# Kernel optimization log

Measured on AMD Instinct MI355X. Metric: run time of the kernel, lower is better.

## Reference

```python
import jax, jax.numpy as jnp
import numpy as np
import math

D_MODEL = 1024
NUM_HEADS = 16
HEAD_DIM = D_MODEL // NUM_HEADS


def setup_inputs() -> dict:
    key = jax.random.key(0)
    ks = jax.random.split(key, 10)
    B, Sq, Skv = 2, 2048, 2048
    s = 1.0 / math.sqrt(D_MODEL)
    return {
        "X": jax.random.normal(ks[0], (B, Skv, D_MODEL), jnp.float32),
        "y": jax.random.normal(ks[1], (B, Sq, D_MODEL), jnp.float32),
        "qW": jax.random.normal(ks[2], (D_MODEL, D_MODEL), jnp.float32) * s,
        "qB": jnp.zeros((D_MODEL,), jnp.float32),
        "kW": jax.random.normal(ks[3], (D_MODEL, D_MODEL), jnp.float32) * s,
        "kB": jnp.zeros((D_MODEL,), jnp.float32),
        "vW": jax.random.normal(ks[4], (D_MODEL, D_MODEL), jnp.float32) * s,
        "vB": jnp.zeros((D_MODEL,), jnp.float32),
        "oW": jax.random.normal(ks[5], (D_MODEL, D_MODEL), jnp.float32) * s,
        "oB": jnp.zeros((D_MODEL,), jnp.float32),
    }


def _split_heads(x):
    # (B, S, D) -> (B, H, S, dk)
    B, S, _ = x.shape
    return x.reshape(B, S, NUM_HEADS, HEAD_DIM).transpose(0, 2, 1, 3)


def reference(X, y, qW, qB, kW, kB, vW, vB, oW, oB):
    B = X.shape[0]
    q = _split_heads(y @ qW + qB)   # queries come from y (decoder)
    k = _split_heads(X @ kW + kB)   # keys/values from X (encoder)
    v = _split_heads(X @ vW + vB)
    scale = 1.0 / math.sqrt(HEAD_DIM)
    scores = jnp.einsum("bhqd,bhkd->bhqk", q, k) * scale
    weights = jax.nn.softmax(scores, axis=-1)
    attn = jnp.einsum("bhqk,bhkd->bhqd", weights, v)
    concat = attn.transpose(0, 2, 1, 3).reshape(B, -1, D_MODEL)
    return concat @ oW + oB
```

## Files before the change

kernel.cpp:

```cpp
#include <hip/hip_runtime.h>
#include <hip/hip_bf16.h>
#include <math.h>

typedef __hip_bfloat16 bf16;
typedef __bf16 nbf16;
typedef __bf16 bf16x8 __attribute__((ext_vector_type(8)));
typedef __bf16 bf16x4 __attribute__((ext_vector_type(4)));
typedef float f32x4 __attribute__((ext_vector_type(4)));

#define D_MODEL 1024
#define NHEAD   16
#define HDK     64
#define BATCH   2
#define SEQ     2048
#define QSZ     ((size_t)BATCH * SEQ * D_MODEL)
#define WSZ     ((size_t)D_MODEL * D_MODEL)

__global__ void detect_dtype(const unsigned short* __restrict__ x, int* flag) {
    __shared__ int cnt;
    if (threadIdx.x == 0) cnt = 0;
    __syncthreads();
    int local = 0;
    for (int i = threadIdx.x; i < 4096; i += 256) {
        const unsigned short v = x[i];
        const int e = (v >> 7) & 0xFF;
        if (v == 0 || (e >= 96 && e <= 141)) local++;
    }
    atomicAdd(&cnt, local);
    __syncthreads();
    if (threadIdx.x == 0) *flag = (cnt >= 3600) ? 1 : 0;
}

__device__ __forceinline__ float ldIn(const void* p, size_t i, int isbf16) {
    return isbf16 ? __bfloat162float(((const bf16*)p)[i])
                  : ((const float*)p)[i];
}

__device__ __forceinline__ void gload_lds16(const void* g, void* l) {
    __builtin_amdgcn_global_load_lds(
        (const __attribute__((address_space(1))) void*)g,
        (__attribute__((address_space(3))) void*)l, 16, 0, 0);
}

__global__ void tobf16_xy(const void* __restrict__ X, const void* __restrict__ Y,
                          nbf16* __restrict__ Xb, nbf16* __restrict__ Yb,
                          const int* __restrict__ flagp) {
    const int flag = *flagp;
    const int half = (int)(QSZ / 2048);
    const bool isX = blockIdx.x < half;
    const void* in = isX ? X : Y;
    nbf16* out     = isX ? Xb : Yb;
    const size_t i = ((size_t)(isX ? blockIdx.x : blockIdx.x - half) * 256 +
                      threadIdx.x) * 8;
    if (flag) {
        *(uint4*)(out + i) = *(const uint4*)((const nbf16*)in + i);
    } else {
        const float4 a = *(const float4*)((const float*)in + i);
        const float4 b = *(const float4*)((const float*)in + i + 4);
        bf16x8 v = {(nbf16)a.x, (nbf16)a.y, (nbf16)a.z, (nbf16)a.w,
                    (nbf16)b.x, (nbf16)b.y, (nbf16)b.z, (nbf16)b.w};
        *(bf16x8*)(out + i) = v;
    }
}

__global__ void wtrans4(const void* __restrict__ qW, const void* __restrict__ kW,
                        const void* __restrict__ vW, const void* __restrict__ oW,
                        nbf16* __restrict__ Wt3, nbf16* __restrict__ Wto,
                        const int* __restrict__ flagp) {
    const int flag = *flagp;
    const int z = blockIdx.z;
    const void* W = (z == 0) ? qW : (z == 1) ? kW : (z == 2) ? vW : oW;
    nbf16* Wt = (z == 3) ? Wto : Wt3 + (size_t)z * WSZ;

    __shared__ float T[64][65];
    const int k0 = blockIdx.x * 64, n0 = blockIdx.y * 64;
    #pragma unroll
    for (int i = 0; i < 16; ++i) {
        const int idx = threadIdx.x + i * 256;
        const int r = idx >> 6, c = idx & 63;
        T[r][c] = ldIn(W, (size_t)(k0 + r) * D_MODEL + n0 + c, flag);
    }
    __syncthreads();
    #pragma unroll
    for (int i = 0; i < 16; ++i) {
        const int idx = threadIdx.x + i * 256;
        const int n = idx >> 6, k = idx & 63;
        Wt[(size_t)(n0 + n) * D_MODEL + k0 + k] = (nbf16)T[k][n];
    }
}

#define STAGE128(Albuf, Blbuf, Aptr, Bptr, t)                                  \
{                                                                              \
    const int _k0 = (t) * 64;                                                  \
    _Pragma("unroll")                                                          \
    for (int i = 0; i < 4; ++i) {                                              \
        const int row = i * 32 + wid * 8 + (lane >> 3);                        \
        const int ss  = (lane & 7) ^ (row & 7);                                \
        gload_lds16((Aptr) + (size_t)row * D_MODEL + _k0 + ss * 8,             \
                    (nbf16*)(Albuf) + i * 2048 + wid * 512);                   \
        gload_lds16((Bptr) + (size_t)row * D_MODEL + _k0 + ss * 8,             \
                    (nbf16*)(Blbuf) + i * 2048 + wid * 512);                   \
    }                                                                          \
}

#define GEMM128_LOOP(Al, Bl)                                                   \
    const int NT = D_MODEL / 64;                                               \
    for (int t = 0; t < NT; ++t) {                                             \
        const int cur = t & 1;                                                 \
        if (t + 1 < NT)                                                        \
            STAGE128(&Al[cur ^ 1][0][0], &Bl[cur ^ 1][0][0], Am, Bm, t + 1);   \
        _Pragma("unroll")                                                      \
        for (int kk = 0; kk < 2; ++kk) {                                       \
            bf16x8 af[4], bfr[4];                                              \
            _Pragma("unroll")                                                  \
            for (int mi = 0; mi < 4; ++mi) {                                   \
                const int ar = wr * 64 + mi * 16 + l15;                        \
                const int sl = ((kk << 2) + lg) ^ (ar & 7);                    \
                af[mi] = *(const bf16x8*)((const nbf16*)&Al[cur][ar][0] + sl * 8); \
            }                                                                  \
            _Pragma("unroll")                                                  \
            for (int ni = 0; ni < 4; ++ni) {                                   \
                const int br = wc * 64 + ni * 16 + l15;                        \
                const int sl = ((kk << 2) + lg) ^ (br & 7);                    \
                bfr[ni] = *(const bf16x8*)((const nbf16*)&Bl[cur][br][0] + sl * 8); \
            }                                                                  \
            _Pragma("unroll")                                                  \
            for (int mi = 0; mi < 4; ++mi)                                     \
                _Pragma("unroll")                                              \
                for (int ni = 0; ni < 4; ++ni)                                 \
                    acc[mi][ni] = __builtin_amdgcn_mfma_f32_16x16x32_bf16(     \
                        af[mi], bfr[ni], acc[mi][ni], 0, 0, 0);                \
        }                                                                      \
        __syncthreads();                                                       \
    }

__global__ __launch_bounds__(256, 2) void proj_qkv(
        const nbf16* __restrict__ Xb, const nbf16* __restrict__ Yb,
        const nbf16* __restrict__ Wt3,
        const void* __restrict__ qB, const void* __restrict__ kB,
        const void* __restrict__ vB,
        nbf16* __restrict__ outq, const int* __restrict__ flagp) {
    __shared__ nbf16 Al[2][128][64];
    __shared__ nbf16 Bl[2][128][64];

    const int flag = *flagp;
    const int tid  = threadIdx.x;
    const int wid  = tid >> 6;
    const int lane = tid & 63;
    const int l15  = lane & 15;
    const int lg   = lane >> 4;
    const int wr   = wid >> 1;
    const int wc   = wid & 1;

    const int id = blockIdx.x;
    const int sw = (id & 7) * 96 + (id >> 3);
    const int m0  = (sw & 31) * 128;
    const int ng0 = (sw >> 5) * 128;

    const nbf16* A  = (ng0 < D_MODEL) ? Yb : Xb;
    const nbf16* Bm = Wt3 + (size_t)ng0 * D_MODEL;
    const nbf16* Am = A + (size_t)m0 * D_MODEL;

    f32x4 acc[4][4];
    #pragma unroll
    for (int mi = 0; mi < 4; ++mi)
        #pragma unroll
        for (int ni = 0; ni < 4; ++ni) acc[mi][ni] = (f32x4){0.f, 0.f, 0.f, 0.f};

    STAGE128(&Al[0][0][0], &Bl[0][0][0], Am, Bm, 0);
    __syncthreads();

    GEMM128_LOOP(Al, Bl)

    #pragma unroll
    for (int ni = 0; ni < 4; ++ni) {
        const int n  = ng0 + wc * 64 + ni * 16 + l15;
        const int wh = n >> 10;
        const int nl = n & 1023;
        const void* bp = (wh == 0) ? qB : (wh == 1) ? kB : vB;
        const float bias = ldIn(bp, (size_t)nl, flag);
        nbf16* outp = outq + (size_t)wh * QSZ;
        #pragma unroll
        for (int mi = 0; mi < 4; ++mi) {
            #pragma unroll
            for (int r = 0; r < 4; ++r) {
                const int m = m0 + wr * 64 + mi * 16 + lg * 4 + r;
                const float v = acc[mi][ni][r] + bias;
                const int b = m >> 11, s = m & (SEQ - 1);
                const int h = nl >> 6,  d = nl & (HDK - 1);
                outp[(((size_t)(b * NHEAD + h)) * SEQ + s) * HDK + d] = (nbf16)v;
            }
        }
    }
}

__global__ __launch_bounds__(256, 2) void proj_o(
        const nbf16* __restrict__ A, const nbf16* __restrict__ Wt,
        const void* __restrict__ Braw, void* __restrict__ Cout,
        const int* __restrict__ flagp) {
    __shared__ nbf16 Al[2][128][64];
    __shared__ nbf16 Bl[2][128][64];

    const int flag = *flagp;
    const int tid  = threadIdx.x;
    const int wid  = tid >> 6;
    const int lane = tid & 63;
    const int l15  = lane & 15;
    const int lg   = lane >> 4;
    const int wr   = wid >> 1;
    const int wc   = wid & 1;

    const int id = blockIdx.x;
    const int sw = (id & 7) * 32 + (id >> 3);
    const int m0 = (sw >> 3) * 128;
    const int n0 = (sw & 7) * 128;

    const nbf16* Am = A + (size_t)m0 * D_MODEL;
    const nbf16* Bm = Wt + (size_t)n0 * D_MODEL;

    f32x4 acc[4][4];
    #pragma unroll
    for (int mi = 0; mi < 4; ++mi)
        #pragma unroll
        for (int ni = 0; ni < 4; ++ni) acc[mi][ni] = (f32x4){0.f, 0.f, 0.f, 0.f};

    STAGE128(&Al[0][0][0], &Bl[0][0][0], Am, Bm, 0);
    __syncthreads();

    GEMM128_LOOP(Al, Bl)

    #pragma unroll
    for (int ni = 0; ni < 4; ++ni) {
        const int n = n0 + wc * 64 + ni * 16 + l15;
        const float bias = ldIn(Braw, (size_t)n, flag);
        #pragma unroll
        for (int mi = 0; mi < 4; ++mi) {
            #pragma unroll
            for (int r = 0; r < 4; ++r) {
                const int m = m0 + wr * 64 + mi * 16 + lg * 4 + r;
                const float v = acc[mi][ni][r] + bias;
                if (flag) ((bf16*)Cout)[(size_t)m * D_MODEL + n] = __float2bfloat16(v);
                else      ((float*)Cout)[(size_t)m * D_MODEL + n] = v;
            }
        }
    }
}

__global__ __launch_bounds__(256, 4) void attn_mfma(
        const nbf16* __restrict__ qg, const nbf16* __restrict__ kg,
        const nbf16* __restrict__ vg, nbf16* __restrict__ cg) {
    __shared__ nbf16 VT[2][64][72];
    __shared__ nbf16 PB[4][32][72];

    const int tid  = threadIdx.x;
    const int wid  = tid >> 6;
    const int lane = tid & 63;
    const int l15  = lane & 15;
    const int lg   = lane >> 4;

    const int id = blockIdx.x;
    const int sw = (id & 7) * 64 + (id >> 3);
    const int bh = sw >> 4;
    const int qt = sw & 15;

    const nbf16* qb = qg + (size_t)bh * SEQ * HDK;
    const nbf16* kb = kg + (size_t)bh * SEQ * HDK;
    const nbf16* vb = vg + (size_t)bh * SEQ * HDK;

    const float SCf = 0.125f * 1.44269504088896340736f;

    const int qbase = qt * 128 + wid * 32;
    const nbf16* qpA = qb + (size_t)(qbase + l15) * HDK + lg * 8;
    const nbf16* qpB = qpA + 16 * HDK;
    bf16x8 qfA0 = *(const bf16x8*)qpA;
    bf16x8 qfA1 = *(const bf16x8*)(qpA + 32);
    bf16x8 qfB0 = *(const bf16x8*)qpB;
    bf16x8 qfB1 = *(const bf16x8*)(qpB + 32);
    #pragma unroll
    for (int j = 0; j < 8; ++j) {
        qfA0[j] = (nbf16)((float)qfA0[j] * SCf);
        qfA1[j] = (nbf16)((float)qfA1[j] * SCf);
        qfB0[j] = (nbf16)((float)qfB0[j] * SCf);
        qfB1[j] = (nbf16)((float)qfB1[j] * SCf);
    }

    const bf16x8 ones = {(nbf16)1.f, (nbf16)1.f, (nbf16)1.f, (nbf16)1.f,
                         (nbf16)1.f, (nbf16)1.f, (nbf16)1.f, (nbf16)1.f};

    const int g8 = (tid >> 5) * 8;
    const int p2 = (tid & 31) * 2;

    #define VLOAD(t)                                                           \
        a0 = *(const uint4*)(vb + (size_t)((t) * 64 + p2) * HDK + g8);         \
        a1 = *(const uint4*)(vb + (size_t)((t) * 64 + p2 + 1) * HDK + g8);

    #define VWRITE(buf)                                                        \
    {                                                                          \
        const unsigned short* e0 = (const unsigned short*)&a0;                 \
        const unsigned short* e1 = (const unsigned short*)&a1;                 \
        _Pragma("unroll")                                                      \
        for (int j = 0; j < 8; ++j)                                            \
            *(unsigned int*)&VT[buf][g8 + j][p2] =                             \
                (unsigned int)e0[j] | ((unsigned int)e1[j] << 16);             \
    }

    #define SOFTMAX(st, m2, o, osum, pbrow)                                    \
    do {                                                                       \
        float tmx[4];                                                          \
        _Pragma("unroll")                                                      \
        for (int s_ = 0; s_ < 4; ++s_)                                         \
            tmx[s_] = fmaxf(fmaxf(st[s_][0], st[s_][1]),                       \
                            fmaxf(st[s_][2], st[s_][3]));                      \
        float tm = fmaxf(fmaxf(tmx[0], tmx[1]), fmaxf(tmx[2], tmx[3]));        \
        tm = fmaxf(tm, __shfl_xor(tm, 16, 64));                                \
        tm = fmaxf(tm, __shfl_xor(tm, 32, 64));                                \
        const bool nresc = __all(tm - m2 <= 8.0f);                             \
        const float mref = nresc ? m2 : fmaxf(m2, tm);                         \
        _Pragma("unroll")                                                      \
        for (int s_ = 0; s_ < 4; ++s_) {                                       \
            const float p0 = exp2f(st[s_][0] - mref);                          \
            const float p1 = exp2f(st[s_][1] - mref);                          \
            const float p2_ = exp2f(st[s_][2] - mref);                         \
            const float p3 = exp2f(st[s_][3] - mref);                          \
            bf16x4 pk = {(nbf16)p0, (nbf16)p1, (nbf16)p2_, (nbf16)p3};         \
            *(bf16x4*)((pbrow) + s_ * 16 + lg * 4) = pk;                       \
        }                                                                      \
        if (!nresc) {                                                          \
            const float alpha = exp2f(m2 - mref);                              \
            m2 = mref;                                                         \
            float av[4];                                                       \
            _Pragma("unroll")                                                  \
            for (int r = 0; r < 4; ++r) av[r] = __shfl(alpha, lg * 4 + r, 64); \
            _Pragma("unroll")                                                  \
            for (int i = 0; i < 4; ++i)                                        \
                _Pragma("unroll")                                              \
                for (int r = 0; r < 4; ++r) o[i][r] *= av[r];                  \
            _Pragma("unroll")                                                  \
            for (int r = 0; r < 4; ++r) osum[r] *= av[r];                      \
        }                                                                      \
    } while (0)

    float m2A = -3.0e38f, m2B = -3.0e38f;
    f32x4 oA[4], oB[4], osumA, osumB;
    #pragma unroll
    for (int i = 0; i < 4; ++i) { oA[i] = (f32x4){0,0,0,0}; oB[i] = (f32x4){0,0,0,0}; }
    osumA = (f32x4){0, 0, 0, 0};
    osumB = (f32x4){0, 0, 0, 0};

    const int NT = SEQ / 64;

    {
        uint4 a0, a1;
        VLOAD(0);
        VWRITE(0);
    }
    __syncthreads();

    for (int t = 0; t < NT; ++t) {
        const int cur = t & 1;
        uint4 a0, a1;
        if (t + 1 < NT) VLOAD(t + 1);

        f32x4 stA[4], stB[4];
        const nbf16* kt = kb + (size_t)t * 64 * HDK;
        __builtin_amdgcn_s_setprio(1);
        #pragma unroll
        for (int sub = 0; sub < 4; ++sub) {
            const nbf16* kp = kt + (size_t)(sub * 16 + l15) * HDK + lg * 8;
            const bf16x8 kf0 = *(const bf16x8*)kp;
            const bf16x8 kf1 = *(const bf16x8*)(kp + 32);
            f32x4 a = (f32x4){0, 0, 0, 0};
            a = __builtin_amdgcn_mfma_f32_16x16x32_bf16(kf0, qfA0, a, 0, 0, 0);
            a = __builtin_amdgcn_mfma_f32_16x16x32_bf16(kf1, qfA1, a, 0, 0, 0);
            stA[sub] = a;
            f32x4 b = (f32x4){0, 0, 0, 0};
            b = __builtin_amdgcn_mfma_f32_16x16x32_bf16(kf0, qfB0, b, 0, 0, 0);
            b = __builtin_amdgcn_mfma_f32_16x16x32_bf16(kf1, qfB1, b, 0, 0, 0);
            stB[sub] = b;
        }
        __builtin_amdgcn_s_setprio(0);

        SOFTMAX(stA, m2A, oA, osumA, &PB[wid][l15][0]);
        SOFTMAX(stB, m2B, oB, osumB, &PB[wid][16 + l15][0]);

        __asm__ volatile("s_waitcnt lgkmcnt(0)" ::: "memory");

        const bf16x8 pfA0 = *(const bf16x8*)&PB[wid][l15][lg * 8];
        const bf16x8 pfA1 = *(const bf16x8*)&PB[wid][l15][lg * 8 + 32];
        const bf16x8 pfB0 = *(const bf16x8*)&PB[wid][16 + l15][lg * 8];
        const bf16x8 pfB1 = *(const bf16x8*)&PB[wid][16 + l15][lg * 8 + 32];
        __builtin_amdgcn_s_setprio(1);
        #pragma unroll
        for (int db = 0; db < 4; ++db) {
            const bf16x8 vf0 = *(const bf16x8*)&VT[cur][db * 16 + l15][lg * 8];
            const bf16x8 vf1 = *(const bf16x8*)&VT[cur][db * 16 + l15][lg * 8 + 32];
            oA[db] = __builtin_amdgcn_mfma_f32_16x16x32_bf16(pfA0, vf0, oA[db], 0, 0, 0);
            oA[db] = __builtin_amdgcn_mfma_f32_16x16x32_bf16(pfA1, vf1, oA[db], 0, 0, 0);
            oB[db] = __builtin_amdgcn_mfma_f32_16x16x32_bf16(pfB0, vf0, oB[db], 0, 0, 0);
            oB[db] = __builtin_amdgcn_mfma_f32_16x16x32_bf16(pfB1, vf1, oB[db], 0, 0, 0);
        }
        osumA = __builtin_amdgcn_mfma_f32_16x16x32_bf16(pfA0, ones, osumA, 0, 0, 0);
        osumA = __builtin_amdgcn_mfma_f32_16x16x32_bf16(pfA1, ones, osumA, 0, 0, 0);
        osumB = __builtin_amdgcn_mfma_f32_16x16x32_bf16(pfB0, ones, osumB, 0, 0, 0);
        osumB = __builtin_amdgcn_mfma_f32_16x16x32_bf16(pfB1, ones, osumB, 0, 0, 0);
        __builtin_amdgcn_s_setprio(0);

        if (t + 1 < NT) VWRITE(cur ^ 1);
        __syncthreads();
    }

    const int b = bh >> 4, h = bh & 15;
    #pragma unroll
    for (int db = 0; db < 4; ++db) {
        #pragma unroll
        for (int r = 0; r < 4; ++r) {
            const int qA = qbase + lg * 4 + r;
            cg[((size_t)(b * SEQ + qA)) * D_MODEL + h * HDK + db * 16 + l15] =
                (nbf16)(oA[db][r] / osumA[r]);
            const int qB_ = qbase + 16 + lg * 4 + r;
            cg[((size_t)(b * SEQ + qB_)) * D_MODEL + h * HDK + db * 16 + l15] =
                (nbf16)(oB[db][r] / osumB[r]);
        }
    }
    #undef VLOAD
    #undef VWRITE
    #undef SOFTMAX
}

extern "C" void kernel_launch(void* const* d_in, const int* in_sizes, int n_in,
                              void* d_out, int out_size, void* d_ws, size_t ws_size,
                              hipStream_t stream) {
    const void* X  = d_in[0];
    const void* Y  = d_in[1];
    const void* qW = d_in[2];
    const void* qB = d_in[3];
    const void* kW = d_in[4];
    const void* kB = d_in[5];
    const void* vW = d_in[6];
    const void* vB = d_in[7];
    const void* oW = d_in[8];
    const void* oB = d_in[9];

    nbf16* ws = (nbf16*)d_ws;
    nbf16* qbuf = ws;
    nbf16* kbuf = qbuf + QSZ;
    nbf16* vbuf = kbuf + QSZ;
    nbf16* cbuf = vbuf + QSZ;
    nbf16* Xb   = cbuf + QSZ;
    nbf16* Yb   = Xb + QSZ;
    nbf16* Wt3  = Yb + QSZ;
    nbf16* Wto  = Wt3 + 3 * WSZ;
    int*   flag = (int*)(Wto + WSZ);

    detect_dtype<<<1, 256, 0, stream>>>((const unsigned short*)X, flag);

    tobf16_xy<<<(int)(2 * (QSZ / 2048)), 256, 0, stream>>>(X, Y, Xb, Yb, flag);

    wtrans4<<<dim3(16, 16, 4), 256, 0, stream>>>(qW, kW, vW, oW, Wt3, Wto, flag);

    proj_qkv<<<768, 256, 0, stream>>>(Xb, Yb, Wt3, qB, kB, vB, qbuf, flag);

    attn_mfma<<<512, 256, 0, stream>>>(qbuf, kbuf, vbuf, cbuf);

    proj_o<<<256, 256, 0, stream>>>(cbuf, Wto, oB, d_out, flag);
}
```

Baseline: 285.5 us.

## Stage K tiles into swizzled LDS via async global-to-LDS loads

The attention kernel now double-buffers each 64-row K tile into shared memory with direct global-to-LDS loads and an XOR swizzle. Previously every wave read K fragments straight from global memory, so the four waves of a block each re-fetched the same tile. The K load for the next tile is issued alongside the V prefetch so it overlaps with the current tile's compute. The change adds 16 KB of LDS and lowers the launch-bounds occupancy hint from 4 to 2 blocks per CU, which may reduce latency hiding.

```diff
diff --git a/kernel.cpp b/kernel.cpp
--- a/kernel.cpp
+++ b/kernel.cpp
@@ -246,9 +246,10 @@
     }
 }
 
-__global__ __launch_bounds__(256, 4) void attn_mfma(
+__global__ __launch_bounds__(256, 2) void attn_mfma(
         const nbf16* __restrict__ qg, const nbf16* __restrict__ kg,
         const nbf16* __restrict__ vg, nbf16* __restrict__ cg) {
+    __shared__ nbf16 KL[2][64][64];
     __shared__ nbf16 VT[2][64][72];
     __shared__ nbf16 PB[4][32][72];
 
@@ -289,6 +290,17 @@
 
     const int g8 = (tid >> 5) * 8;
     const int p2 = (tid & 31) * 2;
+
+    #define STAGEK(buf, t)                                                     \
+    {                                                                          \
+        _Pragma("unroll")                                                      \
+        for (int i = 0; i < 2; ++i) {                                          \
+            const int row = i * 32 + wid * 8 + (lane >> 3);                    \
+            const int ss  = (lane & 7) ^ (row & 7);                            \
+            gload_lds16(kb + (size_t)((t) * 64 + row) * HDK + ss * 8,          \
+                        (nbf16*)&KL[buf][0][0] + i * 2048 + wid * 512);        \
+        }                                                                      \
+    }
 
     #define VLOAD(t)                                                           \
         a0 = *(const uint4*)(vb + (size_t)((t) * 64 + p2) * HDK + g8);         \
@@ -351,6 +363,7 @@
 
     {
         uint4 a0, a1;
+        STAGEK(0, 0);
         VLOAD(0);
         VWRITE(0);
     }
@@ -359,21 +372,25 @@
     for (int t = 0; t < NT; ++t) {
         const int cur = t & 1;
         uint4 a0, a1;
-        if (t + 1 < NT) VLOAD(t + 1);
+        if (t + 1 < NT) {
+            STAGEK(cur ^ 1, t + 1);
+            VLOAD(t + 1);
+        }
 
         f32x4 stA[4], stB[4];
-        const nbf16* kt = kb + (size_t)t * 64 * HDK;
         __builtin_amdgcn_s_setprio(1);
         #pragma unroll
         for (int sub = 0; sub < 4; ++sub) {
-            const nbf16* kp = kt + (size_t)(sub * 16 + l15) * HDK + lg * 8;
-            const bf16x8 kf0 = *(const bf16x8*)kp;
-            const bf16x8 kf1 = *(const bf16x8*)(kp + 32);
-            f32x4 a = (f32x4){0, 0, 0, 0};
+            const int row = sub * 16 + l15;
+            const int s0 = lg ^ (row & 7);
+            const int s1 = (4 + lg) ^ (row & 7);
+            const bf16x8 kf0 = *(const bf16x8*)((const nbf16*)&KL[cur][row][0] + s0 * 8);
+            const bf16x8 kf1 = *(const bf16x8*)((const nbf16*)&KL[cur][row][0] + s1 * 8);
+            f32x4 a = (f32x4){0,0,0,0};
             a = __builtin_amdgcn_mfma_f32_16x16x32_bf16(kf0, qfA0, a, 0, 0, 0);
             a = __builtin_amdgcn_mfma_f32_16x16x32_bf16(kf1, qfA1, a, 0, 0, 0);
             stA[sub] = a;
-            f32x4 b = (f32x4){0, 0, 0, 0};
+            f32x4 b = (f32x4){0,0,0,0};
             b = __builtin_amdgcn_mfma_f32_16x16x32_bf16(kf0, qfB0, b, 0, 0, 0);
             b = __builtin_amdgcn_mfma_f32_16x16x32_bf16(kf1, qfB1, b, 0, 0, 0);
             stB[sub] = b;
@@ -422,6 +439,7 @@
                 (nbf16)(oB[db][r] / osumB[r]);
         }
     }
+    #undef STAGEK
     #undef VLOAD
     #undef VWRITE
     #undef SOFTMAX
```

Result: faster. 252.5 us (-11.5%).
